# Optimization experiments

Measured on AMD Instinct MI355X. Metric: run time of the kernel, lower is better.

## Reference

```python
import jax, jax.numpy as jnp
import numpy as np

M, N, D, P = 16, 2048, 128, 8192
H = N // D  # 16
MAXLEN = 8448
EPS = 1e-5


def layernorm(x, g, b):
    mu = jnp.mean(x, axis=-1, keepdims=True)
    var = jnp.mean(jnp.square(x - mu), axis=-1, keepdims=True)
    return (x - mu) * jax.lax.rsqrt(var + EPS) * g + b


def setup_inputs() -> dict:
    key = jax.random.key(0)
    ks = jax.random.split(key, 10)
    s = 1.0 / np.sqrt(N)  # keep activations O(1) like trained weights
    return {
        "X": jax.random.normal(ks[0], (M, N), jnp.float32),
        "ln1_g": jnp.ones((N,), jnp.float32),
        "ln1_b": jnp.zeros((N,), jnp.float32),
        "Wq": jax.random.normal(ks[1], (N, N), jnp.float32) * s,
        "Wk": jax.random.normal(ks[2], (N, N), jnp.float32) * s,
        "Wv": jax.random.normal(ks[3], (N, N), jnp.float32) * s,
        "Wo": jax.random.normal(ks[4], (N, N), jnp.float32) * s,
        "ln2_g": jnp.ones((N,), jnp.float32),
        "ln2_b": jnp.zeros((N,), jnp.float32),
        "Wup": jax.random.normal(ks[5], (4 * N, N), jnp.float32) * s,
        "Wdown": jax.random.normal(ks[6], (N, 4 * N), jnp.float32) * (1.0 / np.sqrt(4 * N)),
        "cache_K": jax.random.normal(ks[7], (H, MAXLEN, D), jnp.float32),
        "cache_V": jax.random.normal(ks[8], (H, MAXLEN, D), jnp.float32),
    }


def reference(X, ln1_g, ln1_b, Wq, Wk, Wv, Wo, ln2_g, ln2_b, Wup, Wdown, cache_K, cache_V):
    residual = X
    Xn = layernorm(X, ln1_g, ln1_b)
    # torch Linear: y = x @ W.T
    q = (Xn @ Wq.T).reshape(M, H, D).transpose(1, 0, 2)  # (H,M,D)
    k = (Xn @ Wk.T).reshape(M, H, D).transpose(1, 0, 2)
    v = (Xn @ Wv.T).reshape(M, H, D).transpose(1, 0, 2)
    # KV-cache append
    cache_K = jax.lax.dynamic_update_slice(cache_K, k, (0, P, 0))
    cache_V = jax.lax.dynamic_update_slice(cache_V, v, (0, P, 0))
    Kc = cache_K[:, : P + M, :]  # (H,T,D), T = P+M
    Vc = cache_V[:, : P + M, :]
    scores = jnp.einsum("hmd,htd->hmt", q, Kc) / np.sqrt(D)
    weights = jax.nn.softmax(scores, axis=-1)
    attn = jnp.einsum("hmt,htd->hmd", weights, Vc)  # (H,M,D)
    attn = attn.transpose(1, 0, 2).reshape(M, N)
    X = residual + attn @ Wo.T
    residual = X
    Xn = layernorm(X, ln2_g, ln2_b)
    ffn = jax.nn.gelu(Xn @ Wup.T, approximate=False) @ Wdown.T
    return residual + ffn
```

## Files before the change

### kernel.cpp

```cpp
#include <hip/hip_runtime.h>
#include <hip/hip_bf16.h>
#include <math.h>

#define M_TOK 16
#define NDIM  2048
#define DHEAD 128
#define NHEAD 16
#define MAXLEN 8448
#define FFN   8192
#define TC    128
#define NCH   65
#define LN_EPS 1e-5f
#define RSQRT_D 0.08838834764831845f

#define AS1 __attribute__((address_space(1)))
#define AS3 __attribute__((address_space(3)))

typedef float f4v __attribute__((ext_vector_type(4)));
typedef float f2v __attribute__((ext_vector_type(2)));

__device__ __forceinline__ void gload_lds16(const float* g, float* l) {
    __builtin_amdgcn_global_load_lds((AS1 void*)g, (AS3 void*)l, 16, 0, 0);
}

__device__ __forceinline__ uint32_t lds_off(const void* p) {
    return (uint32_t)(uintptr_t)(const AS3 void*)p;
}

__device__ __forceinline__ f4v dsr_b128(uint32_t off) {
    f4v r; asm volatile("ds_read_b128 %0, %1" : "=v"(r) : "v"(off)); return r;
}
__device__ __forceinline__ f2v dsr_b64(uint32_t off) {
    f2v r; asm volatile("ds_read_b64 %0, %1" : "=v"(r) : "v"(off)); return r;
}
__device__ __forceinline__ float dsr_b32(uint32_t off) {
    float r; asm volatile("ds_read_b32 %0, %1" : "=v"(r) : "v"(off)); return r;
}
__device__ __forceinline__ void dsw_b32(uint32_t off, float v) {
    asm volatile("ds_write_b32 %0, %1" : : "v"(off), "v"(v));
}
#define LGKM0()  asm volatile("s_waitcnt lgkmcnt(0)" ::: "memory")
#define SCHED0() __builtin_amdgcn_sched_barrier(0)

template<int H>
__device__ __forceinline__ void fold_step(float* v, int lane, int o) {
    bool hi = (lane & o) != 0;
    #pragma unroll
    for (int i = 0; i < H; ++i) {
        float send = hi ? v[i] : v[i + H];
        float keep = hi ? v[i + H] : v[i];
        v[i] = keep + __shfl_xor(send, o);
    }
}

__device__ __forceinline__ void fold32(float* v, int lane) {
    fold_step<16>(v, lane, 32);
    fold_step<8>(v, lane, 16);
    fold_step<4>(v, lane, 8);
    fold_step<2>(v, lane, 4);
    fold_step<1>(v, lane, 2);
    v[0] += __shfl_xor(v[0], 1);
}

template<int KDIM>
__device__ __forceinline__ void gemv_core8(const float* __restrict__ A,
                                           const float* __restrict__ W,
                                           int cb, int w, int lane,
                                           float* sbuf, float* acc) {
    constexpr int NS = KDIM / 256;
    const float* wsrc0 = W + (size_t)(cb + 2 * w)     * KDIM + lane * 4;
    const float* wsrc1 = W + (size_t)(cb + 2 * w + 1) * KDIM + lane * 4;
    auto issue = [&](int s) {
        if (s >= NS) return;
        float* dst = sbuf + (s % 3) * 6144;
        gload_lds16(wsrc0 + s * 256, dst + (2 * w) * 256);
        gload_lds16(wsrc1 + s * 256, dst + (2 * w + 1) * 256);
        #pragma unroll
        for (int j = 0; j < 4; ++j) {
            int m = w * 4 + j;
            gload_lds16(A + (size_t)m * KDIM + s * 256 + lane * 4,
                        dst + 2048 + m * 256);
        }
    };
    issue(0); issue(1); issue(2);
    const uint32_t sb = lds_off(sbuf);
    #pragma unroll 1
    for (int s = 0; s < NS; ++s) {
        int rem = NS - 1 - s;
        if (rem >= 2)      asm volatile("s_waitcnt vmcnt(12)" ::: "memory");
        else if (rem == 1) asm volatile("s_waitcnt vmcnt(6)" ::: "memory");
        else               asm volatile("s_waitcnt vmcnt(0)" ::: "memory");
        __builtin_amdgcn_s_barrier();
        SCHED0();
        uint32_t b = sb + (uint32_t)((s % 3) * 6144) * 4u;
        f4v wr0 = dsr_b128(b + (uint32_t)((2 * w) * 256 + lane * 4) * 4u);
        f4v wr1 = dsr_b128(b + (uint32_t)((2 * w + 1) * 256 + lane * 4) * 4u);
        f4v xr[16];
        #pragma unroll
        for (int m = 0; m < 16; ++m)
            xr[m] = dsr_b128(b + (uint32_t)(2048 + m * 256 + lane * 4) * 4u);
        LGKM0();
        SCHED0();
        __builtin_amdgcn_s_barrier();
        issue(s + 3);
        #pragma unroll
        for (int m = 0; m < 16; ++m) {
            acc[m*2]   = fmaf(wr0.x, xr[m].x, acc[m*2]);
            acc[m*2]   = fmaf(wr0.y, xr[m].y, acc[m*2]);
            acc[m*2]   = fmaf(wr0.z, xr[m].z, acc[m*2]);
            acc[m*2]   = fmaf(wr0.w, xr[m].w, acc[m*2]);
            acc[m*2+1] = fmaf(wr1.x, xr[m].x, acc[m*2+1]);
            acc[m*2+1] = fmaf(wr1.y, xr[m].y, acc[m*2+1]);
            acc[m*2+1] = fmaf(wr1.z, xr[m].z, acc[m*2+1]);
            acc[m*2+1] = fmaf(wr1.w, xr[m].w, acc[m*2+1]);
        }
    }
}

__global__ __launch_bounds__(256) void k_qkv(const float* __restrict__ Xn,
                                             const float* __restrict__ Wq,
                                             const float* __restrict__ Wk,
                                             const float* __restrict__ Wv,
                                             float* __restrict__ qws,
                                             float* __restrict__ kws,
                                             float* __restrict__ vws) {
    __shared__ float sbuf[3 * 6144];
    int tid = threadIdx.x, w = tid >> 6, lane = tid & 63;
    int b = blockIdx.x;
    int sel = b >> 8;
    int cb = (b & 255) * 8;
    const float* W = (sel == 0) ? Wq : (sel == 1) ? Wk : Wv;
    float* dst = (sel == 0) ? qws : (sel == 1) ? kws : vws;
    float acc[32];
    #pragma unroll
    for (int i = 0; i < 32; ++i) acc[i] = 0.f;
    gemv_core8<2048>(Xn, W, cb, w, lane, sbuf, acc);
    fold32(acc, lane);
    if ((lane & 1) == 0) {
        int idx = (lane >> 1) & 31;
        int m = idx >> 1, c = idx & 1;
        int gcol = cb + 2 * w + c;
        int hh = gcol >> 7, d = gcol & 127;
        dst[(((size_t)hh * 16 + m) << 7) + d] = acc[0];
    }
}

__device__ __forceinline__ float gelu_exact(float x) {
    return 0.5f * x * (1.0f + erff(x * 0.7071067811865475f));
}

__global__ __launch_bounds__(256) void k_up(const float* __restrict__ A,
                                            const float* __restrict__ W,
                                            float* __restrict__ out) {
    __shared__ float sbuf[3 * 6144];
    int tid = threadIdx.x, w = tid >> 6, lane = tid & 63;
    int cb = blockIdx.x * 8;
    float acc[32];
    #pragma unroll
    for (int i = 0; i < 32; ++i) acc[i] = 0.f;
    gemv_core8<2048>(A, W, cb, w, lane, sbuf, acc);
    fold32(acc, lane);
    if ((lane & 1) == 0) {
        int idx = (lane >> 1) & 31;
        int m = idx >> 1, c = idx & 1;
        out[(size_t)m * FFN + cb + 2 * w + c] = gelu_exact(acc[0]);
    }
}

template<int KDIM>
__global__ __launch_bounds__(256) void k_resid(const float* __restrict__ A,
                                               const float* __restrict__ W,
                                               const float* __restrict__ R,
                                               float* __restrict__ out) {
    __shared__ float sbuf[3 * 6144];
    int tid = threadIdx.x, w = tid >> 6, lane = tid & 63;
    int cb = blockIdx.x * 8;
    float acc[32];
    #pragma unroll
    for (int i = 0; i < 32; ++i) acc[i] = 0.f;
    gemv_core8<KDIM>(A, W, cb, w, lane, sbuf, acc);
    fold32(acc, lane);
    if ((lane & 1) == 0) {
        int idx = (lane >> 1) & 31;
        int m = idx >> 1, c = idx & 1;
        int col = cb + 2 * w + c;
        out[(size_t)m * NDIM + col] = R[(size_t)m * NDIM + col] + acc[0];
    }
}

__global__ __launch_bounds__(256) void k_ln(const float* __restrict__ X,
                                            const float* __restrict__ g,
                                            const float* __restrict__ b,
                                            float* __restrict__ out) {
    int row = blockIdx.x, tid = threadIdx.x;
    const float4* xp = (const float4*)(X + (size_t)row * NDIM);
    float4 v0 = xp[tid], v1 = xp[tid + 256];
    float s = v0.x + v0.y + v0.z + v0.w + v1.x + v1.y + v1.z + v1.w;
    float q = v0.x*v0.x + v0.y*v0.y + v0.z*v0.z + v0.w*v0.w
            + v1.x*v1.x + v1.y*v1.y + v1.z*v1.z + v1.w*v1.w;
    #pragma unroll
    for (int o = 32; o; o >>= 1) { s += __shfl_xor(s, o); q += __shfl_xor(q, o); }
    __shared__ float ls[4], lq[4];
    int wid = tid >> 6, lane = tid & 63;
    if (lane == 0) { ls[wid] = s; lq[wid] = q; }
    __syncthreads();
    s = ls[0] + ls[1] + ls[2] + ls[3];
    q = lq[0] + lq[1] + lq[2] + lq[3];
    float mu  = s * (1.f / NDIM);
    float var = q * (1.f / NDIM) - mu * mu;
    float rs  = rsqrtf(var + LN_EPS);
    float4 g0 = ((const float4*)g)[tid], g1 = ((const float4*)g)[tid + 256];
    float4 b0 = ((const float4*)b)[tid], b1 = ((const float4*)b)[tid + 256];
    float4 o0, o1;
    o0.x = (v0.x - mu) * rs * g0.x + b0.x;  o0.y = (v0.y - mu) * rs * g0.y + b0.y;
    o0.z = (v0.z - mu) * rs * g0.z + b0.z;  o0.w = (v0.w - mu) * rs * g0.w + b0.w;
    o1.x = (v1.x - mu) * rs * g1.x + b1.x;  o1.y = (v1.y - mu) * rs * g1.y + b1.y;
    o1.z = (v1.z - mu) * rs * g1.z + b1.z;  o1.w = (v1.w - mu) * rs * g1.w + b1.w;
    float4* op = (float4*)(out + (size_t)row * NDIM);
    op[tid] = o0; op[tid + 256] = o1;
}

__global__ __launch_bounds__(256, 2) void k_attn(const float* __restrict__ cacheK,
                                                 const float* __restrict__ cacheV,
                                                 const float* __restrict__ qws,
                                                 const float* __restrict__ kws,
                                                 const float* __restrict__ vws,
                                                 float* __restrict__ part,
                                                 float* __restrict__ ms) {
    __shared__ float s_k[4][2080];
    __shared__ float s_v[4][2080];
    __shared__ float s_p[16][132];
    int bid = blockIdx.x;
    int h = bid / NCH, c = bid % NCH;
    int nT = (c < NCH - 1) ? TC : M_TOK;
    int NST = nT >> 4;
    const float* Kb = (c < NCH - 1) ? cacheK + ((size_t)h * MAXLEN + (size_t)c * TC) * DHEAD
                                    : kws + (size_t)h * M_TOK * DHEAD;
    const float* Vb = (c < NCH - 1) ? cacheV + ((size_t)h * MAXLEN + (size_t)c * TC) * DHEAD
                                    : vws + (size_t)h * M_TOK * DHEAD;
    int tid = threadIdx.x, w = tid >> 6, lane = tid & 63;
    int tloc = lane & 15, ds = lane >> 4;

    float4 qreg[4][8];
    {
        const float4* qp = (const float4*)(qws + (size_t)h * M_TOK * DHEAD);
        #pragma unroll
        for (int mm = 0; mm < 4; ++mm) {
            #pragma unroll
            for (int i = 0; i < 8; ++i)
                qreg[mm][i] = qp[(size_t)(w * 4 + mm) * 32 + ds * 8 + i];
        }
    }
    asm volatile("s_waitcnt vmcnt(0)" ::: "memory");

    auto issue = [&](int slot) {
        if (slot >= 2 * NST) return;
        const float* src; float* dst;
        if (slot < NST) { src = Kb + (size_t)slot * 16 * DHEAD; dst = s_k[slot & 3]; }
        else { int j = slot - NST; src = Vb + (size_t)j * 16 * DHEAD; dst = s_v[j & 3]; }
        #pragma unroll
        for (int k = 0; k < 2; ++k) {
            int j = w * 2 + k;
            gload_lds16(src + j * 256 + lane * 4, dst + j * 260);
        }
    };

    issue(0); issue(1); issue(2); issue(3);
    const int lastSlot = 2 * NST - 1;
    const uint32_t skb = lds_off(s_k);
    const uint32_t svb = lds_off(s_v);
    const uint32_t spb = lds_off(s_p);

    #define WAIT_LADDER(s)                                                     \
        { int rem = lastSlot - (s);                                            \
          if (rem >= 3)      asm volatile("s_waitcnt vmcnt(6)" ::: "memory");  \
          else if (rem == 2) asm volatile("s_waitcnt vmcnt(4)" ::: "memory");  \
          else if (rem == 1) asm volatile("s_waitcnt vmcnt(2)" ::: "memory");  \
          else               asm volatile("s_waitcnt vmcnt(0)" ::: "memory"); }

    for (int s = 0; s < NST; ++s) {
        WAIT_LADDER(s);
        __builtin_amdgcn_s_barrier();
        SCHED0();
        uint32_t kb = skb + (uint32_t)((s & 3) * 2080 +
                     (tloc >> 1) * 260 + (tloc & 1) * 128 + ds * 32) * 4u;
        f4v kr[8];
        #pragma unroll
        for (int i = 0; i < 8; ++i) kr[i] = dsr_b128(kb + i * 16);
        LGKM0();
        SCHED0();
        __builtin_amdgcn_s_barrier();
        issue(s + 4);
        #pragma unroll
        for (int mm = 0; mm < 4; ++mm) {
            float a0 = 0.f, a1 = 0.f, a2 = 0.f, a3 = 0.f;
            #pragma unroll
            for (int i = 0; i < 8; ++i) {
                a0 = fmaf(kr[i].x, qreg[mm][i].x, a0);
                a1 = fmaf(kr[i].y, qreg[mm][i].y, a1);
                a2 = fmaf(kr[i].z, qreg[mm][i].z, a2);
                a3 = fmaf(kr[i].w, qreg[mm][i].w, a3);
            }
            float s0 = (a0 + a1) + (a2 + a3);
            s0 += __shfl_xor(s0, 16);
            s0 += __shfl_xor(s0, 32);
            if (ds == 0)
                dsw_b32(spb + (uint32_t)((w * 4 + mm) * 132 + s * 16 + tloc) * 4u,
                        s0 * RSQRT_D);
        }
    }

    LGKM0();
    SCHED0();
    float sm_mx, sm_sum;
    int m2 = tid >> 4, tl = tid & 15;
    {
        uint32_t prow = spb + (uint32_t)(m2 * 132) * 4u;
        float mx = -1e30f;
        for (int t = tl; t < nT; t += 16) mx = fmaxf(mx, dsr_b32(prow + t * 4));
        LGKM0();
        #pragma unroll
        for (int o = 8; o; o >>= 1) mx = fmaxf(mx, __shfl_xor(mx, o));
        float sm = 0.f;
        for (int t = tl; t < nT; t += 16) {
            float p = __expf(dsr_b32(prow + t * 4) - mx);
            LGKM0();
            dsw_b32(prow + t * 4, p);
            sm += p;
        }
        #pragma unroll
        for (int o = 8; o; o >>= 1) sm += __shfl_xor(sm, o);
        sm_mx = mx; sm_sum = sm;
    }
    LGKM0();
    SCHED0();

    float2 acc[4] = {{0.f,0.f},{0.f,0.f},{0.f,0.f},{0.f,0.f}};
    for (int j = 0; j < NST; ++j) {
        int s = NST + j;
        WAIT_LADDER(s);
        __builtin_amdgcn_s_barrier();
        SCHED0();
        uint32_t vb = svb + (uint32_t)((j & 3) * 2080) * 4u;
        f2v vr[16];
        #pragma unroll
        for (int r = 0; r < 16; ++r)
            vr[r] = dsr_b64(vb + (uint32_t)((r >> 1) * 260 + (r & 1) * 128 + lane * 2) * 4u);
        f4v p0[4], p1[4], p2[4], p3[4];
        #pragma unroll
        for (int mm = 0; mm < 4; ++mm) {
            uint32_t prow = spb + (uint32_t)((w * 4 + mm) * 132 + j * 16) * 4u;
            p0[mm] = dsr_b128(prow);
            p1[mm] = dsr_b128(prow + 16);
            p2[mm] = dsr_b128(prow + 32);
            p3[mm] = dsr_b128(prow + 48);
        }
        LGKM0();
        SCHED0();
        __builtin_amdgcn_s_barrier();
        issue(s + 4);
        #pragma unroll
        for (int mm = 0; mm < 4; ++mm) {
            acc[mm].x = fmaf(p0[mm].x, vr[0].x, acc[mm].x);
            acc[mm].y = fmaf(p0[mm].x, vr[0].y, acc[mm].y);
            acc[mm].x = fmaf(p0[mm].y, vr[1].x, acc[mm].x);
            acc[mm].y = fmaf(p0[mm].y, vr[1].y, acc[mm].y);
            acc[mm].x = fmaf(p0[mm].z, vr[2].x, acc[mm].x);
            acc[mm].y = fmaf(p0[mm].z, vr[2].y, acc[mm].y);
            acc[mm].x = fmaf(p0[mm].w, vr[3].x, acc[mm].x);
            acc[mm].y = fmaf(p0[mm].w, vr[3].y, acc[mm].y);
            acc[mm].x = fmaf(p1[mm].x, vr[4].x, acc[mm].x);
            acc[mm].y = fmaf(p1[mm].x, vr[4].y, acc[mm].y);
            acc[mm].x = fmaf(p1[mm].y, vr[5].x, acc[mm].x);
            acc[mm].y = fmaf(p1[mm].y, vr[5].y, acc[mm].y);
            acc[mm].x = fmaf(p1[mm].z, vr[6].x, acc[mm].x);
            acc[mm].y = fmaf(p1[mm].z, vr[6].y, acc[mm].y);
            acc[mm].x = fmaf(p1[mm].w, vr[7].x, acc[mm].x);
            acc[mm].y = fmaf(p1[mm].w, vr[7].y, acc[mm].y);
            acc[mm].x = fmaf(p2[mm].x, vr[8].x, acc[mm].x);
            acc[mm].y = fmaf(p2[mm].x, vr[8].y, acc[mm].y);
            acc[mm].x = fmaf(p2[mm].y, vr[9].x, acc[mm].x);
            acc[mm].y = fmaf(p2[mm].y, vr[9].y, acc[mm].y);
            acc[mm].x = fmaf(p2[mm].z, vr[10].x, acc[mm].x);
            acc[mm].y = fmaf(p2[mm].z, vr[10].y, acc[mm].y);
            acc[mm].x = fmaf(p2[mm].w, vr[11].x, acc[mm].x);
            acc[mm].y = fmaf(p2[mm].w, vr[11].y, acc[mm].y);
            acc[mm].x = fmaf(p3[mm].x, vr[12].x, acc[mm].x);
            acc[mm].y = fmaf(p3[mm].x, vr[12].y, acc[mm].y);
            acc[mm].x = fmaf(p3[mm].y, vr[13].x, acc[mm].x);
            acc[mm].y = fmaf(p3[mm].y, vr[13].y, acc[mm].y);
            acc[mm].x = fmaf(p3[mm].z, vr[14].x, acc[mm].x);
            acc[mm].y = fmaf(p3[mm].z, vr[14].y, acc[mm].y);
            acc[mm].x = fmaf(p3[mm].w, vr[15].x, acc[mm].x);
            acc[mm].y = fmaf(p3[mm].w, vr[15].y, acc[mm].y);
        }
    }
    #undef WAIT_LADDER

    float* dp = part + (((size_t)(h * NCH + c) * 16) + w * 4) * DHEAD + 2 * lane;
    #pragma unroll
    for (int mm = 0; mm < 4; ++mm)
        *(float2*)(dp + (size_t)mm * DHEAD) = acc[mm];
    if (tl == 0) {
        float* msp = ms + ((size_t)(h * NCH + c) * 16 + m2) * 2;
        msp[0] = sm_mx; msp[1] = sm_sum;
    }
}

__global__ __launch_bounds__(256) void k_combine(const float* __restrict__ part,
                                                 const float* __restrict__ ms,
                                                 float* __restrict__ attnout) {
    __shared__ float s_scale[16][NCH + 3];
    int h = blockIdx.x >> 3, dblk = blockIdx.x & 7;
    int tid = threadIdx.x;
    {
        int cl = tid & 15, m = tid >> 4;
        float gmax = -1e30f;
        for (int c = cl; c < NCH; c += 16)
            gmax = fmaxf(gmax, ms[((size_t)(h * NCH + c) * 16 + m) * 2]);
        #pragma unroll
        for (int o = 8; o; o >>= 1) gmax = fmaxf(gmax, __shfl_xor(gmax, o));
        float denom = 0.f;
        for (int c = cl; c < NCH; c += 16) {
            const float* msp = ms + ((size_t)(h * NCH + c) * 16 + m) * 2;
            denom += msp[1] * __expf(msp[0] - gmax);
        }
        #pragma unroll
        for (int o = 8; o; o >>= 1) denom += __shfl_xor(denom, o);
        float inv = 1.f / denom;
        for (int c = cl; c < NCH; c += 16) {
            const float* msp = ms + ((size_t)(h * NCH + c) * 16 + m) * 2;
            s_scale[m][c] = __expf(msp[0] - gmax) * inv;
        }
    }
    __syncthreads();
    int m = tid >> 4, dd = tid & 15;
    int d = dblk * 16 + dd;
    const float* pp = part + ((size_t)h * NCH * 16 + m) * DHEAD + d;
    float acc = 0.f;
    #pragma unroll 4
    for (int c = 0; c < NCH; ++c)
        acc = fmaf(pp[(size_t)c * 16 * DHEAD], s_scale[m][c], acc);
    attnout[(size_t)m * NDIM + h * DHEAD + d] = acc;
}

extern "C" void kernel_launch(void* const* d_in, const int* in_sizes, int n_in,
                              void* d_out, int out_size, void* d_ws, size_t ws_size,
                              hipStream_t stream) {
    const float* X      = (const float*)d_in[0];
    const float* ln1_g  = (const float*)d_in[1];
    const float* ln1_b  = (const float*)d_in[2];
    const float* Wq     = (const float*)d_in[3];
    const float* Wk     = (const float*)d_in[4];
    const float* Wv     = (const float*)d_in[5];
    const float* Wo     = (const float*)d_in[6];
    const float* ln2_g  = (const float*)d_in[7];
    const float* ln2_b  = (const float*)d_in[8];
    const float* Wup    = (const float*)d_in[9];
    const float* Wdown  = (const float*)d_in[10];
    const float* cacheK = (const float*)d_in[11];
    const float* cacheV = (const float*)d_in[12];
    float* out = (float*)d_out;

    float* ws = (float*)d_ws;
    float* Xn1    = ws;
    float* qws    = Xn1 + 32768;
    float* kws    = qws + 32768;
    float* vws    = kws + 32768;
    float* partb  = vws + 32768;
    float* msb    = partb + 2129920;
    float* attn_o = msb + 33280;
    float* X2     = attn_o + 32768;
    float* Xn2    = X2 + 32768;
    float* ffnh   = Xn2 + 32768;

    k_ln<<<M_TOK, 256, 0, stream>>>(X, ln1_g, ln1_b, Xn1);
    k_qkv<<<768, 256, 0, stream>>>(Xn1, Wq, Wk, Wv, qws, kws, vws);
    k_attn<<<NHEAD * NCH, 256, 0, stream>>>(cacheK, cacheV, qws, kws, vws, partb, msb);
    k_combine<<<NHEAD * 8, 256, 0, stream>>>(partb, msb, attn_o);
    k_resid<2048><<<256, 256, 0, stream>>>(attn_o, Wo, X, X2);
    k_ln<<<M_TOK, 256, 0, stream>>>(X2, ln2_g, ln2_b, Xn2);
    k_up<<<1024, 256, 0, stream>>>(Xn2, Wup, ffnh);
    k_resid<8192><<<256, 256, 0, stream>>>(ffnh, Wdown, X2, out);
}
```

Before: 142.5 us.

## Rewrite split-KV attention with bf16 MFMA and smaller swizzled chunks

The attention kernel now computes QK^T and PV with 16x16x32 bf16 MFMA instructions instead of scalar FP32 FMAs. Chunk size is halved to 64 tokens, doubling the number of blocks, and each chunk's whole K/V tile is loaded into XOR-swizzled LDS in one pass rather than through the old 4-slot streaming pipeline. The aim is to cut VALU work and raise parallelism on what is a memory-bound cache scan. In exchange it doubles the partial-output and combine traffic and rounds Q, K, P and V to bf16, which lowers accuracy.

```diff
diff --git a/kernel.cpp b/kernel.cpp
--- a/kernel.cpp
+++ b/kernel.cpp
@@ -8,8 +8,8 @@
 #define NHEAD 16
 #define MAXLEN 8448
 #define FFN   8192
-#define TC    128
-#define NCH   65
+#define TC    64
+#define NCH   129
 #define LN_EPS 1e-5f
 #define RSQRT_D 0.08838834764831845f
 
@@ -18,6 +18,7 @@
 
 typedef float f4v __attribute__((ext_vector_type(4)));
 typedef float f2v __attribute__((ext_vector_type(2)));
+typedef short bf16x8 __attribute__((ext_vector_type(8)));
 
 __device__ __forceinline__ void gload_lds16(const float* g, float* l) {
     __builtin_amdgcn_global_load_lds((AS1 void*)g, (AS3 void*)l, 16, 0, 0);
@@ -30,17 +31,27 @@
 __device__ __forceinline__ f4v dsr_b128(uint32_t off) {
     f4v r; asm volatile("ds_read_b128 %0, %1" : "=v"(r) : "v"(off)); return r;
 }
-__device__ __forceinline__ f2v dsr_b64(uint32_t off) {
-    f2v r; asm volatile("ds_read_b64 %0, %1" : "=v"(r) : "v"(off)); return r;
-}
 __device__ __forceinline__ float dsr_b32(uint32_t off) {
     float r; asm volatile("ds_read_b32 %0, %1" : "=v"(r) : "v"(off)); return r;
 }
 __device__ __forceinline__ void dsw_b32(uint32_t off, float v) {
     asm volatile("ds_write_b32 %0, %1" : : "v"(off), "v"(v));
 }
+__device__ __forceinline__ f4v gload_b128(const float* p) {
+    f4v r;
+    asm volatile("global_load_dwordx4 %0, %1, off"
+                 : "=v"(r) : "v"((unsigned long long)(uintptr_t)p));
+    return r;
+}
 #define LGKM0()  asm volatile("s_waitcnt lgkmcnt(0)" ::: "memory")
+#define VM0()    asm volatile("s_waitcnt vmcnt(0)" ::: "memory")
 #define SCHED0() __builtin_amdgcn_sched_barrier(0)
+
+__device__ __forceinline__ short f2bf(float x) {
+    unsigned u = __float_as_uint(x);
+    unsigned r = u + 0x7fffu + ((u >> 16) & 1u);
+    return (short)(r >> 16);
+}
 
 template<int H>
 __device__ __forceinline__ void fold_step(float* v, int lane, int o) {
@@ -220,187 +231,188 @@
     op[tid] = o0; op[tid + 256] = o1;
 }
 
-__global__ __launch_bounds__(256, 2) void k_attn(const float* __restrict__ cacheK,
-                                                 const float* __restrict__ cacheV,
-                                                 const float* __restrict__ qws,
-                                                 const float* __restrict__ kws,
-                                                 const float* __restrict__ vws,
-                                                 float* __restrict__ part,
-                                                 float* __restrict__ ms) {
-    __shared__ float s_k[4][2080];
-    __shared__ float s_v[4][2080];
-    __shared__ float s_p[16][132];
+__global__ __launch_bounds__(256) void k_attn(const float* __restrict__ cacheK,
+                                              const float* __restrict__ cacheV,
+                                              const float* __restrict__ qws,
+                                              const float* __restrict__ kws,
+                                              const float* __restrict__ vws,
+                                              float* __restrict__ part,
+                                              float* __restrict__ ms) {
+    __shared__ float s_k[TC * DHEAD];
+    __shared__ float s_v[TC * DHEAD];
+    __shared__ float s_p[16 * 68];
     int bid = blockIdx.x;
     int h = bid / NCH, c = bid % NCH;
     int nT = (c < NCH - 1) ? TC : M_TOK;
-    int NST = nT >> 4;
+    bool full = (nT == TC);
+    int nSeg = nT >> 1;
     const float* Kb = (c < NCH - 1) ? cacheK + ((size_t)h * MAXLEN + (size_t)c * TC) * DHEAD
                                     : kws + (size_t)h * M_TOK * DHEAD;
     const float* Vb = (c < NCH - 1) ? cacheV + ((size_t)h * MAXLEN + (size_t)c * TC) * DHEAD
                                     : vws + (size_t)h * M_TOK * DHEAD;
     int tid = threadIdx.x, w = tid >> 6, lane = tid & 63;
-    int tloc = lane & 15, ds = lane >> 4;
-
-    float4 qreg[4][8];
-    {
-        const float4* qp = (const float4*)(qws + (size_t)h * M_TOK * DHEAD);
-        #pragma unroll
-        for (int mm = 0; mm < 4; ++mm) {
-            #pragma unroll
-            for (int i = 0; i < 8; ++i)
-                qreg[mm][i] = qp[(size_t)(w * 4 + mm) * 32 + ds * 8 + i];
-        }
-    }
-    asm volatile("s_waitcnt vmcnt(0)" ::: "memory");
-
-    auto issue = [&](int slot) {
-        if (slot >= 2 * NST) return;
-        const float* src; float* dst;
-        if (slot < NST) { src = Kb + (size_t)slot * 16 * DHEAD; dst = s_k[slot & 3]; }
-        else { int j = slot - NST; src = Vb + (size_t)j * 16 * DHEAD; dst = s_v[j & 3]; }
-        #pragma unroll
-        for (int k = 0; k < 2; ++k) {
-            int j = w * 2 + k;
-            gload_lds16(src + j * 256 + lane * 4, dst + j * 260);
-        }
-    };
-
-    issue(0); issue(1); issue(2); issue(3);
-    const int lastSlot = 2 * NST - 1;
+    int g = lane >> 4;
+
+    #pragma unroll
+    for (int k = 0; k < 8; ++k) {
+        int j = w + 4 * k;
+        if (j < nSeg) {
+            int b = j * 1024 + lane * 16;
+            int src = b ^ (((b >> 9) & 7) << 4);
+            gload_lds16(Kb + (src >> 2), s_k + j * 256);
+        }
+    }
+
+    int m_l = lane & 15;
+    const float* qbase = qws + (size_t)h * M_TOK * DHEAD + (size_t)m_l * DHEAD;
+    f4v qlo[4], qhi[4];
+    #pragma unroll
+    for (int blk = 0; blk < 4; ++blk) {
+        qlo[blk] = gload_b128(qbase + blk * 32 + g * 4);
+        qhi[blk] = gload_b128(qbase + blk * 32 + g * 4 + 16);
+    }
+    VM0();
+    SCHED0();
+
+    bf16x8 qf[4];
+    #pragma unroll
+    for (int blk = 0; blk < 4; ++blk) {
+        qf[blk][0] = f2bf(qlo[blk].x); qf[blk][1] = f2bf(qlo[blk].y);
+        qf[blk][2] = f2bf(qlo[blk].z); qf[blk][3] = f2bf(qlo[blk].w);
+        qf[blk][4] = f2bf(qhi[blk].x); qf[blk][5] = f2bf(qhi[blk].y);
+        qf[blk][6] = f2bf(qhi[blk].z); qf[blk][7] = f2bf(qhi[blk].w);
+    }
+
+    #pragma unroll
+    for (int k = 0; k < 8; ++k) {
+        int j = w + 4 * k;
+        if (j < nSeg) {
+            int b = j * 1024 + lane * 16;
+            int src = b ^ (((b >> 9) & 7) << 4);
+            gload_lds16(Vb + (src >> 2), s_v + j * 256);
+        }
+    }
+    __builtin_amdgcn_s_barrier();
+
     const uint32_t skb = lds_off(s_k);
     const uint32_t svb = lds_off(s_v);
     const uint32_t spb = lds_off(s_p);
 
-    #define WAIT_LADDER(s)                                                     \
-        { int rem = lastSlot - (s);                                            \
-          if (rem >= 3)      asm volatile("s_waitcnt vmcnt(6)" ::: "memory");  \
-          else if (rem == 2) asm volatile("s_waitcnt vmcnt(4)" ::: "memory");  \
-          else if (rem == 1) asm volatile("s_waitcnt vmcnt(2)" ::: "memory");  \
-          else               asm volatile("s_waitcnt vmcnt(0)" ::: "memory"); }
-
-    for (int s = 0; s < NST; ++s) {
-        WAIT_LADDER(s);
-        __builtin_amdgcn_s_barrier();
-        SCHED0();
-        uint32_t kb = skb + (uint32_t)((s & 3) * 2080 +
-                     (tloc >> 1) * 260 + (tloc & 1) * 128 + ds * 32) * 4u;
-        f4v kr[8];
-        #pragma unroll
-        for (int i = 0; i < 8; ++i) kr[i] = dsr_b128(kb + i * 16);
+    int t0 = w * 16;
+    if (t0 < nT) {
+        int trow = t0 + (lane & 15);
+        uint32_t xo = (uint32_t)((trow & 7) << 4);
+        f4v klo[4], khi[4];
+        #pragma unroll
+        for (int blk = 0; blk < 4; ++blk) {
+            uint32_t base = (uint32_t)(trow * 512 + blk * 128 + g * 16);
+            klo[blk] = dsr_b128(skb + ((base)      ^ xo));
+            khi[blk] = dsr_b128(skb + ((base + 64) ^ xo));
+        }
         LGKM0();
         SCHED0();
-        __builtin_amdgcn_s_barrier();
-        issue(s + 4);
-        #pragma unroll
-        for (int mm = 0; mm < 4; ++mm) {
-            float a0 = 0.f, a1 = 0.f, a2 = 0.f, a3 = 0.f;
-            #pragma unroll
-            for (int i = 0; i < 8; ++i) {
-                a0 = fmaf(kr[i].x, qreg[mm][i].x, a0);
-                a1 = fmaf(kr[i].y, qreg[mm][i].y, a1);
-                a2 = fmaf(kr[i].z, qreg[mm][i].z, a2);
-                a3 = fmaf(kr[i].w, qreg[mm][i].w, a3);
-            }
-            float s0 = (a0 + a1) + (a2 + a3);
-            s0 += __shfl_xor(s0, 16);
-            s0 += __shfl_xor(s0, 32);
-            if (ds == 0)
-                dsw_b32(spb + (uint32_t)((w * 4 + mm) * 132 + s * 16 + tloc) * 4u,
-                        s0 * RSQRT_D);
-        }
-    }
-
+        f4v accS = {0.f, 0.f, 0.f, 0.f};
+        #pragma unroll
+        for (int blk = 0; blk < 4; ++blk) {
+            bf16x8 bk;
+            bk[0] = f2bf(klo[blk].x); bk[1] = f2bf(klo[blk].y);
+            bk[2] = f2bf(klo[blk].z); bk[3] = f2bf(klo[blk].w);
+            bk[4] = f2bf(khi[blk].x); bk[5] = f2bf(khi[blk].y);
+            bk[6] = f2bf(khi[blk].z); bk[7] = f2bf(khi[blk].w);
+            accS = __builtin_amdgcn_mfma_f32_16x16x32_bf16(qf[blk], bk, accS, 0, 0, 0);
+        }
+        #pragma unroll
+        for (int r = 0; r < 4; ++r) {
+            int m = g * 4 + r;
+            dsw_b32(spb + (uint32_t)((m * 68 + t0 + (lane & 15)) * 4), accS[r] * RSQRT_D);
+        }
+    }
     LGKM0();
-    SCHED0();
+    __builtin_amdgcn_s_barrier();
+
+    int m2 = tid >> 4, tl = tid & 15;
     float sm_mx, sm_sum;
-    int m2 = tid >> 4, tl = tid & 15;
     {
-        uint32_t prow = spb + (uint32_t)(m2 * 132) * 4u;
-        float mx = -1e30f;
-        for (int t = tl; t < nT; t += 16) mx = fmaxf(mx, dsr_b32(prow + t * 4));
-        LGKM0();
-        #pragma unroll
-        for (int o = 8; o; o >>= 1) mx = fmaxf(mx, __shfl_xor(mx, o));
-        float sm = 0.f;
-        for (int t = tl; t < nT; t += 16) {
-            float p = __expf(dsr_b32(prow + t * 4) - mx);
-            LGKM0();
-            dsw_b32(prow + t * 4, p);
-            sm += p;
-        }
-        #pragma unroll
-        for (int o = 8; o; o >>= 1) sm += __shfl_xor(sm, o);
-        sm_mx = mx; sm_sum = sm;
-    }
-    LGKM0();
-    SCHED0();
-
-    float2 acc[4] = {{0.f,0.f},{0.f,0.f},{0.f,0.f},{0.f,0.f}};
-    for (int j = 0; j < NST; ++j) {
-        int s = NST + j;
-        WAIT_LADDER(s);
-        __builtin_amdgcn_s_barrier();
-        SCHED0();
-        uint32_t vb = svb + (uint32_t)((j & 3) * 2080) * 4u;
-        f2v vr[16];
-        #pragma unroll
-        for (int r = 0; r < 16; ++r)
-            vr[r] = dsr_b64(vb + (uint32_t)((r >> 1) * 260 + (r & 1) * 128 + lane * 2) * 4u);
-        f4v p0[4], p1[4], p2[4], p3[4];
-        #pragma unroll
-        for (int mm = 0; mm < 4; ++mm) {
-            uint32_t prow = spb + (uint32_t)((w * 4 + mm) * 132 + j * 16) * 4u;
-            p0[mm] = dsr_b128(prow);
-            p1[mm] = dsr_b128(prow + 16);
-            p2[mm] = dsr_b128(prow + 32);
-            p3[mm] = dsr_b128(prow + 48);
+        uint32_t prow = spb + (uint32_t)(m2 * 68 * 4);
+        float r0 = dsr_b32(prow + (uint32_t)(tl * 4));
+        float r1 = -1e30f, r2 = -1e30f, r3 = -1e30f;
+        if (full) {
+            r1 = dsr_b32(prow + (uint32_t)((tl + 16) * 4));
+            r2 = dsr_b32(prow + (uint32_t)((tl + 32) * 4));
+            r3 = dsr_b32(prow + (uint32_t)((tl + 48) * 4));
         }
         LGKM0();
         SCHED0();
+        float mx = fmaxf(fmaxf(r0, r1), fmaxf(r2, r3));
+        #pragma unroll
+        for (int o = 8; o; o >>= 1) mx = fmaxf(mx, __shfl_xor(mx, o));
+        float p0 = __expf(r0 - mx), sum = p0;
+        dsw_b32(prow + (uint32_t)(tl * 4), p0);
+        if (full) {
+            float p1 = __expf(r1 - mx), p2 = __expf(r2 - mx), p3 = __expf(r3 - mx);
+            sum += p1 + p2 + p3;
+            dsw_b32(prow + (uint32_t)((tl + 16) * 4), p1);
+            dsw_b32(prow + (uint32_t)((tl + 32) * 4), p2);
+            dsw_b32(prow + (uint32_t)((tl + 48) * 4), p3);
+        }
+        #pragma unroll
+        for (int o = 8; o; o >>= 1) sum += __shfl_xor(sum, o);
+        sm_mx = mx; sm_sum = sum;
+    }
+    LGKM0();
+    VM0();
+    __builtin_amdgcn_s_barrier();
+
+    if (!full) {
+        for (int i = tid; i < 16 * 128; i += 256) {
+            int r = 16 + (i >> 7), dd = i & 127;
+            dsw_b32(svb + (uint32_t)((r * 512 + dd * 4) ^ ((r & 7) << 4)), 0.f);
+        }
+        { int m = tid >> 4, t = 16 + (tid & 15);
+          dsw_b32(spb + (uint32_t)((m * 68 + t) * 4), 0.f); }
+        LGKM0();
         __builtin_amdgcn_s_barrier();
-        issue(s + 4);
-        #pragma unroll
-        for (int mm = 0; mm < 4; ++mm) {
-            acc[mm].x = fmaf(p0[mm].x, vr[0].x, acc[mm].x);
-            acc[mm].y = fmaf(p0[mm].x, vr[0].y, acc[mm].y);
-            acc[mm].x = fmaf(p0[mm].y, vr[1].x, acc[mm].x);
-            acc[mm].y = fmaf(p0[mm].y, vr[1].y, acc[mm].y);
-            acc[mm].x = fmaf(p0[mm].z, vr[2].x, acc[mm].x);
-            acc[mm].y = fmaf(p0[mm].z, vr[2].y, acc[mm].y);
-            acc[mm].x = fmaf(p0[mm].w, vr[3].x, acc[mm].x);
-            acc[mm].y = fmaf(p0[mm].w, vr[3].y, acc[mm].y);
-            acc[mm].x = fmaf(p1[mm].x, vr[4].x, acc[mm].x);
-            acc[mm].y = fmaf(p1[mm].x, vr[4].y, acc[mm].y);
-            acc[mm].x = fmaf(p1[mm].y, vr[5].x, acc[mm].x);
-            acc[mm].y = fmaf(p1[mm].y, vr[5].y, acc[mm].y);
-            acc[mm].x = fmaf(p1[mm].z, vr[6].x, acc[mm].x);
-            acc[mm].y = fmaf(p1[mm].z, vr[6].y, acc[mm].y);
-            acc[mm].x = fmaf(p1[mm].w, vr[7].x, acc[mm].x);
-            acc[mm].y = fmaf(p1[mm].w, vr[7].y, acc[mm].y);
-            acc[mm].x = fmaf(p2[mm].x, vr[8].x, acc[mm].x);
-            acc[mm].y = fmaf(p2[mm].x, vr[8].y, acc[mm].y);
-            acc[mm].x = fmaf(p2[mm].y, vr[9].x, acc[mm].x);
-            acc[mm].y = fmaf(p2[mm].y, vr[9].y, acc[mm].y);
-            acc[mm].x = fmaf(p2[mm].z, vr[10].x, acc[mm].x);
-            acc[mm].y = fmaf(p2[mm].z, vr[10].y, acc[mm].y);
-            acc[mm].x = fmaf(p2[mm].w, vr[11].x, acc[mm].x);
-            acc[mm].y = fmaf(p2[mm].w, vr[11].y, acc[mm].y);
-            acc[mm].x = fmaf(p3[mm].x, vr[12].x, acc[mm].x);
-            acc[mm].y = fmaf(p3[mm].x, vr[12].y, acc[mm].y);
-            acc[mm].x = fmaf(p3[mm].y, vr[13].x, acc[mm].x);
-            acc[mm].y = fmaf(p3[mm].y, vr[13].y, acc[mm].y);
-            acc[mm].x = fmaf(p3[mm].z, vr[14].x, acc[mm].x);
-            acc[mm].y = fmaf(p3[mm].z, vr[14].y, acc[mm].y);
-            acc[mm].x = fmaf(p3[mm].w, vr[15].x, acc[mm].x);
-            acc[mm].y = fmaf(p3[mm].w, vr[15].y, acc[mm].y);
-        }
-    }
-    #undef WAIT_LADDER
-
-    float* dp = part + (((size_t)(h * NCH + c) * 16) + w * 4) * DHEAD + 2 * lane;
-    #pragma unroll
-    for (int mm = 0; mm < 4; ++mm)
-        *(float2*)(dp + (size_t)mm * DHEAD) = acc[mm];
+    }
+
+    f4v accO0 = {0.f,0.f,0.f,0.f}, accO1 = {0.f,0.f,0.f,0.f};
+    int dc0 = w * 32 + (lane & 15);
+    int nTC = (nT + 31) >> 5;
+    #pragma unroll
+    for (int tc = 0; tc < 2; ++tc) {
+        if (tc >= nTC) break;
+        int m = lane & 15;
+        f4v plo = dsr_b128(spb + (uint32_t)((m * 68 + tc * 32 + g * 4) * 4));
+        f4v phi = dsr_b128(spb + (uint32_t)((m * 68 + tc * 32 + g * 4 + 16) * 4));
+        float va[8], vb_[8];
+        #pragma unroll
+        for (int half = 0; half < 2; ++half) {
+            #pragma unroll
+            for (int jj = 0; jj < 4; ++jj) {
+                int t = tc * 32 + g * 4 + jj + half * 16;
+                uint32_t xo = (uint32_t)((t & 7) << 4);
+                va[half*4+jj]  = dsr_b32(svb + ((uint32_t)(t * 512 + dc0 * 4)        ^ xo));
+                vb_[half*4+jj] = dsr_b32(svb + ((uint32_t)(t * 512 + (dc0+16) * 4)   ^ xo));
+            }
+        }
+        LGKM0();
+        SCHED0();
+        bf16x8 pa;
+        pa[0] = f2bf(plo.x); pa[1] = f2bf(plo.y); pa[2] = f2bf(plo.z); pa[3] = f2bf(plo.w);
+        pa[4] = f2bf(phi.x); pa[5] = f2bf(phi.y); pa[6] = f2bf(phi.z); pa[7] = f2bf(phi.w);
+        bf16x8 v0, v1;
+        #pragma unroll
+        for (int j = 0; j < 8; ++j) { v0[j] = f2bf(va[j]); v1[j] = f2bf(vb_[j]); }
+        accO0 = __builtin_amdgcn_mfma_f32_16x16x32_bf16(pa, v0, accO0, 0, 0, 0);
+        accO1 = __builtin_amdgcn_mfma_f32_16x16x32_bf16(pa, v1, accO1, 0, 0, 0);
+    }
+
+    float* pb = part + ((size_t)(h * NCH + c) * 16) * DHEAD;
+    #pragma unroll
+    for (int r = 0; r < 4; ++r) {
+        int m = g * 4 + r;
+        pb[(size_t)m * DHEAD + dc0]      = accO0[r];
+        pb[(size_t)m * DHEAD + dc0 + 16] = accO1[r];
+    }
     if (tl == 0) {
         float* msp = ms + ((size_t)(h * NCH + c) * 16 + m2) * 2;
         msp[0] = sm_mx; msp[1] = sm_sum;
@@ -468,8 +480,8 @@
     float* kws    = qws + 32768;
     float* vws    = kws + 32768;
     float* partb  = vws + 32768;
-    float* msb    = partb + 2129920;
-    float* attn_o = msb + 33280;
+    float* msb    = partb + 4227072;
+    float* attn_o = msb + 66048;
     float* X2     = attn_o + 32768;
     float* Xn2    = X2 + 32768;
     float* ffnh   = Xn2 + 32768;
```

Result: no change. 141.8 us (-0.5%).
